# Kernel optimization log

Measured on AMD Instinct MI355X. Metric: run time of the kernel, lower is better.

## Reference

```python
import jax, jax.numpy as jnp
import numpy as np

B, S, D = 32, 1024, 1025  # batch, seq_length(=num_loci), input_dim
QD, KD = 64, 64
INIT_SCALE = 0.03


def _attention(y, Wq, Wk, Wv):
    # y: [B, S, D]
    q = jnp.einsum('bsd,dq->bsq', y, Wq)
    k = jnp.einsum('bsd,dk->bsk', y, Wk)
    v = jnp.einsum('bsd,de->bse', y, Wv)
    scores = jax.nn.softmax(jnp.einsum('bsq,btq->bst', q, k), axis=-1)
    return jnp.einsum('bst,bte->bse', scores, v)


def setup_inputs() -> dict:
    key = jax.random.key(0)
    ks = jax.random.split(key, 13)
    p = lambda k, shape: INIT_SCALE * jax.random.normal(k, shape, dtype=jnp.float32)
    return {
        'x': jax.random.normal(ks[0], (B, S, D), dtype=jnp.float32),
        'Wq1': p(ks[1], (D, QD)), 'Wk1': p(ks[2], (D, KD)), 'Wv1': p(ks[3], (D, D)),
        'Wq2': p(ks[4], (D, QD)), 'Wk2': p(ks[5], (D, KD)), 'Wv2': p(ks[6], (D, D)),
        'Wq3': p(ks[7], (D, QD)), 'Wk3': p(ks[8], (D, KD)), 'Wv3': p(ks[9], (D, D)),
        'random_matrix': p(ks[10], (S, D - 1)),
        'coeffs_attended': p(ks[11], (S, D)),
        'offset': p(ks[12], (1,)),
    }


def reference(x, Wq1, Wk1, Wv1, Wq2, Wk2, Wv2, Wq3, Wk3, Wv3,
              random_matrix, coeffs_attended, offset):
    # y = concat(x[:, :, :S] @ random_matrix, x[:, :, -1:])  -> [B, S, D]
    y = jnp.concatenate(
        [jnp.einsum('bsf,fe->bse', x[:, :, :S], random_matrix), x[:, :, -1:]],
        axis=2)
    a1 = _attention(y, Wq1, Wk1, Wv1)
    a2 = _attention(a1, Wq2, Wk2, Wv2)
    a3 = _attention(a2, Wq3, Wk3, Wv3)
    out = jnp.einsum('bij,ij->b', a3, coeffs_attended) + offset
    return out
```

## Files before the change

### kernel.cpp

```cpp
#include <hip/hip_runtime.h>
#include <hip/hip_bf16.h>
#include <stdint.h>

typedef __bf16 bf16;
typedef __bf16 bf16x8 __attribute__((ext_vector_type(8)));
typedef float f32x4 __attribute__((ext_vector_type(4)));
typedef float f32x8u __attribute__((ext_vector_type(8)));
typedef f32x8u f32x8a __attribute__((aligned(4)));

__device__ __forceinline__ void gl16(const void* g, void* lds) {
  __builtin_amdgcn_global_load_lds(
      (const __attribute__((address_space(1))) void*)g,
      (__attribute__((address_space(3))) void*)lds, 16, 0, 0);
}

template <int OUT>
__global__ __launch_bounds__(256) void gemm_hr(
    const bf16* __restrict__ Ah, const bf16* __restrict__ Ar, int lda,
    long long sA_, const bf16* __restrict__ Bh, const bf16* __restrict__ Br,
    int ldb, long long sB_, float* __restrict__ Cf, bf16* __restrict__ Ch,
    bf16* __restrict__ Cr, int ldc, long long sC_, int N, int K, int ntn) {
  __shared__ bf16 tAh[128][32], tAr[128][32], tBh[128][32], tBr[128][32];

  const int tid = threadIdx.x;
  const int lane = tid & 63, wave = tid >> 6;
  const int wm = wave & 1, wn = wave >> 1;
  const int fr = lane & 15, fq = lane >> 4;

  const long long bz = blockIdx.y;
  Ah += bz * sA_;
  Ar += bz * sA_;
  Bh += bz * sB_;
  Br += bz * sB_;

  const int cpx = gridDim.x >> 3;
  const int b2 = (blockIdx.x & 7) * cpx + (blockIdx.x >> 3);
  const int tm = b2 / ntn, tn = b2 % ntn;
  const int m0 = tm * 128, n0 = tn * 128;

  const int c0 = wave * 128 + lane;
  const int colsw = (((c0 & 3) ^ ((c0 >> 3) & 3)) << 3);
  const int rA0 = m0 + (c0 >> 2);
  int rB0 = n0 + (c0 >> 2), rB1 = rB0 + 16;
  rB0 = rB0 < N ? rB0 : N - 1;
  rB1 = rB1 < N ? rB1 : N - 1;
  const long long offA0 = (long long)rA0 * lda + colsw;
  const long long offA1 = offA0 + (long long)16 * lda;
  const long long offB0 = (long long)rB0 * ldb + colsw;
  const long long offB1 = (long long)rB1 * ldb + colsw;

  char* dAh = (char*)&tAh[0][0] + wave * 2048;
  char* dAr = (char*)&tAr[0][0] + wave * 2048;
  char* dBh = (char*)&tBh[0][0] + wave * 2048;
  char* dBr = (char*)&tBr[0][0] + wave * 2048;

  const int colA = ((fq ^ ((fr >> 1) & 3)) << 3);

  f32x4 acc[4][4] = {};
  const int nk = K >> 5;
  for (int kt = 0; kt < nk; ++kt) {
    const int k0 = kt << 5;
    gl16(Ah + offA0 + k0, dAh);
    gl16(Ah + offA1 + k0, dAh + 1024);
    gl16(Ar + offA0 + k0, dAr);
    gl16(Ar + offA1 + k0, dAr + 1024);
    gl16(Bh + offB0 + k0, dBh);
    gl16(Bh + offB1 + k0, dBh + 1024);
    gl16(Br + offB0 + k0, dBr);
    gl16(Br + offB1 + k0, dBr + 1024);
    __syncthreads();

    bf16x8 ah[4], ar_[4], bh[4], br_[4];
#pragma unroll
    for (int i = 0; i < 4; ++i) {
      ah[i] = *reinterpret_cast<const bf16x8*>(&tAh[wm * 64 + i * 16 + fr][colA]);
      ar_[i] = *reinterpret_cast<const bf16x8*>(&tAr[wm * 64 + i * 16 + fr][colA]);
      bh[i] = *reinterpret_cast<const bf16x8*>(&tBh[wn * 64 + i * 16 + fr][colA]);
      br_[i] = *reinterpret_cast<const bf16x8*>(&tBr[wn * 64 + i * 16 + fr][colA]);
    }
#pragma unroll
    for (int mi = 0; mi < 4; ++mi)
#pragma unroll
      for (int ni = 0; ni < 4; ++ni)
        acc[mi][ni] = __builtin_amdgcn_mfma_f32_16x16x32_bf16(
            ah[mi], bh[ni], acc[mi][ni], 0, 0, 0);
#pragma unroll
    for (int mi = 0; mi < 4; ++mi)
#pragma unroll
      for (int ni = 0; ni < 4; ++ni)
        acc[mi][ni] = __builtin_amdgcn_mfma_f32_16x16x32_bf16(
            ah[mi], br_[ni], acc[mi][ni], 0, 0, 0);
#pragma unroll
    for (int mi = 0; mi < 4; ++mi)
#pragma unroll
      for (int ni = 0; ni < 4; ++ni)
        acc[mi][ni] = __builtin_amdgcn_mfma_f32_16x16x32_bf16(
            ar_[mi], bh[ni], acc[mi][ni], 0, 0, 0);
    __syncthreads();
  }

  if constexpr (OUT == 0) {
    float* C = Cf + bz * sC_;
#pragma unroll
    for (int mi = 0; mi < 4; ++mi)
#pragma unroll
      for (int ni = 0; ni < 4; ++ni) {
        int cc = n0 + wn * 64 + ni * 16 + fr;
        if (cc < N) {
          long long base = (long long)(m0 + wm * 64 + mi * 16 + fq * 4) * ldc + cc;
#pragma unroll
          for (int j = 0; j < 4; ++j) C[base + (long long)j * ldc] = acc[mi][ni][j];
        }
      }
  } else {
    bf16* CH = Ch + bz * sC_;
    bf16* CR = Cr + bz * sC_;
#pragma unroll
    for (int mi = 0; mi < 4; ++mi)
#pragma unroll
      for (int ni = 0; ni < 4; ++ni) {
        int cc = n0 + wn * 64 + ni * 16 + fr;
        if (cc < N) {
          long long base = (long long)(m0 + wm * 64 + mi * 16 + fq * 4) * ldc + cc;
#pragma unroll
          for (int j = 0; j < 4; ++j) {
            float v = acc[mi][ni][j];
            bf16 h = (bf16)v;
            CH[base + (long long)j * ldc] = h;
            CR[base + (long long)j * ldc] = (bf16)(v - (float)h);
          }
        }
      }
  }
}

template <int OUT>
__global__ __launch_bounds__(256, 2) void gemm_hr2(
    const bf16* __restrict__ Ah, const bf16* __restrict__ Ar, int lda,
    long long sA_, const bf16* __restrict__ Bh, const bf16* __restrict__ Br,
    int ldb, long long sB_, float* __restrict__ Cf, bf16* __restrict__ Ch,
    bf16* __restrict__ Cr, int ldc, long long sC_, int N, int K, int ntn) {
  __shared__ bf16 tAh[256][32], tAr[256][32], tBh[128][32], tBr[128][32];

  const int tid = threadIdx.x;
  const int lane = tid & 63, wave = tid >> 6;
  const int wm = wave & 1, wn = wave >> 1;
  const int fr = lane & 15, fq = lane >> 4;

  const long long bz = blockIdx.y;
  Ah += bz * sA_;
  Ar += bz * sA_;
  Bh += bz * sB_;
  Br += bz * sB_;

  const int nwg = gridDim.x;
  const int q = nwg >> 3, r = nwg & 7;
  const int xcd = blockIdx.x & 7, o8 = blockIdx.x >> 3;
  const int b2 = (xcd < r ? xcd * (q + 1) : r * (q + 1) + (xcd - r) * q) + o8;
  const int tm = b2 / ntn, tn = b2 % ntn;
  const int m0 = tm * 256, n0 = tn * 128;

  const int cA = wave * 64 + lane;
  const int colsw = (((cA & 3) ^ ((cA >> 3) & 3)) << 3);
  const int rA = cA >> 2;
  const long long offA = (long long)(m0 + rA) * lda + colsw;
  const long long strA = (long long)64 * lda;
  int rB0 = n0 + rA, rB1 = n0 + rA + 64;
  rB0 = rB0 < N ? rB0 : N - 1;
  rB1 = rB1 < N ? rB1 : N - 1;
  const long long offB0 = (long long)rB0 * ldb + colsw;
  const long long offB1 = (long long)rB1 * ldb + colsw;

  char* dAh = (char*)&tAh[0][0] + wave * 1024;
  char* dAr = (char*)&tAr[0][0] + wave * 1024;
  char* dBh = (char*)&tBh[0][0] + wave * 1024;
  char* dBr = (char*)&tBr[0][0] + wave * 1024;

  const int colA = ((fq ^ ((fr >> 1) & 3)) << 3);

  f32x4 acc[8][4] = {};
  const int nk = K >> 5;
  for (int kt = 0; kt < nk; ++kt) {
    const int k0 = kt << 5;
#pragma unroll
    for (int j = 0; j < 4; ++j) {
      gl16(Ah + offA + j * strA + k0, dAh + j * 4096);
      gl16(Ar + offA + j * strA + k0, dAr + j * 4096);
    }
    gl16(Bh + offB0 + k0, dBh);
    gl16(Bh + offB1 + k0, dBh + 4096);
    gl16(Br + offB0 + k0, dBr);
    gl16(Br + offB1 + k0, dBr + 4096);
    __syncthreads();

    bf16x8 bh[4], br_[4];
#pragma unroll
    for (int i = 0; i < 4; ++i) {
      bh[i] = *reinterpret_cast<const bf16x8*>(&tBh[wn * 64 + i * 16 + fr][colA]);
      br_[i] = *reinterpret_cast<const bf16x8*>(&tBr[wn * 64 + i * 16 + fr][colA]);
    }
#pragma unroll
    for (int mi = 0; mi < 8; ++mi) {
      bf16x8 ah = *reinterpret_cast<const bf16x8*>(
          &tAh[wm * 128 + mi * 16 + fr][colA]);
      bf16x8 ar_ = *reinterpret_cast<const bf16x8*>(
          &tAr[wm * 128 + mi * 16 + fr][colA]);
#pragma unroll
      for (int ni = 0; ni < 4; ++ni)
        acc[mi][ni] = __builtin_amdgcn_mfma_f32_16x16x32_bf16(
            ah, bh[ni], acc[mi][ni], 0, 0, 0);
#pragma unroll
      for (int ni = 0; ni < 4; ++ni)
        acc[mi][ni] = __builtin_amdgcn_mfma_f32_16x16x32_bf16(
            ah, br_[ni], acc[mi][ni], 0, 0, 0);
#pragma unroll
      for (int ni = 0; ni < 4; ++ni)
        acc[mi][ni] = __builtin_amdgcn_mfma_f32_16x16x32_bf16(
            ar_, bh[ni], acc[mi][ni], 0, 0, 0);
    }
    __syncthreads();
  }

  if constexpr (OUT == 0) {
    float* C = Cf + bz * sC_;
#pragma unroll
    for (int mi = 0; mi < 8; ++mi)
#pragma unroll
      for (int ni = 0; ni < 4; ++ni) {
        int cc = n0 + wn * 64 + ni * 16 + fr;
        if (cc < N) {
          long long base =
              (long long)(m0 + wm * 128 + mi * 16 + fq * 4) * ldc + cc;
#pragma unroll
          for (int j = 0; j < 4; ++j) C[base + (long long)j * ldc] = acc[mi][ni][j];
        }
      }
  } else if constexpr (OUT == 1) {
    bf16* CH = Ch + bz * sC_;
    bf16* CR = Cr + bz * sC_;
#pragma unroll
    for (int mi = 0; mi < 8; ++mi)
#pragma unroll
      for (int ni = 0; ni < 4; ++ni) {
        int cc = n0 + wn * 64 + ni * 16 + fr;
        if (cc < N) {
          long long base =
              (long long)(m0 + wm * 128 + mi * 16 + fq * 4) * ldc + cc;
#pragma unroll
          for (int j = 0; j < 4; ++j) {
            float v = acc[mi][ni][j];
            bf16 h = (bf16)v;
            CH[base + (long long)j * ldc] = h;
            CR[base + (long long)j * ldc] = (bf16)(v - (float)h);
          }
        }
      }
  } else {
    bf16* CH = Ch + bz * sC_;
    bf16* CR = Cr + bz * sC_;
#pragma unroll
    for (int mi = 0; mi < 8; ++mi)
#pragma unroll
      for (int ni = 0; ni < 4; ++ni) {
        int cc = n0 + wn * 64 + ni * 16 + fr;
        if (cc < N) {
          int mr = m0 + wm * 128 + mi * 16 + fq * 4;
          union { bf16 h[4]; uint2 u; } th, tr;
#pragma unroll
          for (int j = 0; j < 4; ++j) {
            float v = acc[mi][ni][j];
            bf16 h = (bf16)v;
            th.h[j] = h;
            tr.h[j] = (bf16)(v - (float)h);
          }
          *reinterpret_cast<uint2*>(CH + (long long)cc * ldc + mr) = th.u;
          *reinterpret_cast<uint2*>(CR + (long long)cc * ldc + mr) = tr.u;
        }
      }
  }
}

__global__ __launch_bounds__(256, 2) void gemm_dot1(
    const bf16* __restrict__ Ah, int lda, long long sA_,
    const bf16* __restrict__ Bh, int ldb, long long sB_, int N, int K,
    int ntn, const float* __restrict__ G, int ldg,
    float* __restrict__ partial) {
  __shared__ bf16 tAh[256][32], tBh[128][32];

  const int tid = threadIdx.x;
  const int lane = tid & 63, wave = tid >> 6;
  const int wm = wave & 1, wn = wave >> 1;
  const int fr = lane & 15, fq = lane >> 4;

  const long long bz = blockIdx.y;
  Ah += bz * sA_;
  Bh += bz * sB_;

  const int nwg = gridDim.x;
  const int q = nwg >> 3, r = nwg & 7;
  const int xcd = blockIdx.x & 7, o8 = blockIdx.x >> 3;
  const int b2 = (xcd < r ? xcd * (q + 1) : r * (q + 1) + (xcd - r) * q) + o8;
  const int tm = b2 / ntn, tn = b2 % ntn;
  const int m0 = tm * 256, n0 = tn * 128;

  const int cA = wave * 64 + lane;
  const int colsw = (((cA & 3) ^ ((cA >> 3) & 3)) << 3);
  const int rA = cA >> 2;
  const long long offA = (long long)(m0 + rA) * lda + colsw;
  const long long strA = (long long)64 * lda;
  int rB0 = n0 + rA, rB1 = n0 + rA + 64;
  rB0 = rB0 < N ? rB0 : N - 1;
  rB1 = rB1 < N ? rB1 : N - 1;
  const long long offB0 = (long long)rB0 * ldb + colsw;
  const long long offB1 = (long long)rB1 * ldb + colsw;

  char* dAh = (char*)&tAh[0][0] + wave * 1024;
  char* dBh = (char*)&tBh[0][0] + wave * 1024;

  const int colA = ((fq ^ ((fr >> 1) & 3)) << 3);

  f32x4 acc[8][4] = {};
  const int nk = K >> 5;
  for (int kt = 0; kt < nk; ++kt) {
    const int k0 = kt << 5;
#pragma unroll
    for (int j = 0; j < 4; ++j) gl16(Ah + offA + j * strA + k0, dAh + j * 4096);
    gl16(Bh + offB0 + k0, dBh);
    gl16(Bh + offB1 + k0, dBh + 4096);
    __syncthreads();

    bf16x8 bh[4];
#pragma unroll
    for (int i = 0; i < 4; ++i)
      bh[i] = *reinterpret_cast<const bf16x8*>(&tBh[wn * 64 + i * 16 + fr][colA]);
#pragma unroll
    for (int mi = 0; mi < 8; ++mi) {
      bf16x8 ah = *reinterpret_cast<const bf16x8*>(
          &tAh[wm * 128 + mi * 16 + fr][colA]);
#pragma unroll
      for (int ni = 0; ni < 4; ++ni)
        acc[mi][ni] = __builtin_amdgcn_mfma_f32_16x16x32_bf16(
            ah, bh[ni], acc[mi][ni], 0, 0, 0);
    }
    __syncthreads();
  }

  float dot = 0.f;
#pragma unroll
  for (int mi = 0; mi < 8; ++mi)
#pragma unroll
    for (int ni = 0; ni < 4; ++ni) {
      int cc = n0 + wn * 64 + ni * 16 + fr;
      if (cc < N) {
        long long base =
            (long long)(m0 + wm * 128 + mi * 16 + fq * 4) * ldg + cc;
#pragma unroll
        for (int j = 0; j < 4; ++j)
          dot += acc[mi][ni][j] * G[base + (long long)j * ldg];
      }
    }
#pragma unroll
  for (int o = 32; o; o >>= 1) dot += __shfl_xor(dot, o);
  float* red = (float*)&tAh[0][0];
  if (lane == 0) red[wave] = dot;
  __syncthreads();
  if (tid == 0)
    partial[bz * gridDim.x + b2] = red[0] + red[1] + red[2] + red[3];
}

__global__ __launch_bounds__(256) void gemm0_split(
    const float* __restrict__ A, int lda, const float* __restrict__ B, int ldb,
    bf16* __restrict__ Ch, bf16* __restrict__ Cr, int ldc, int N, int K,
    int ntn) {
  __shared__ bf16 tAh[128][32], tAr[128][32], tBh[128][32], tBr[128][32];

  const int tid = threadIdx.x;
  const int lane = tid & 63, wave = tid >> 6;
  const int wm = wave & 1, wn = wave >> 1;
  const int fr = lane & 15, fq = lane >> 4;

  const int cpx = gridDim.x >> 3;
  const int b2 = (blockIdx.x & 7) * cpx + (blockIdx.x >> 3);
  const int tm = b2 / ntn, tn = b2 % ntn;
  const int m0 = tm * 128, n0 = tn * 128;

  const int row0 = tid >> 2, slot = tid & 3;
  const int wcol = ((slot ^ ((tid >> 3) & 3)) << 3);
  const int colA = ((fq ^ ((fr >> 1) & 3)) << 3);

  f32x4 acc[4][4] = {};
  const int nk = K >> 5;
  for (int kt = 0; kt < nk; ++kt) {
    const int k0 = kt << 5;
    f32x8a ra[2], rb[2];
#pragma unroll
    for (int p = 0; p < 2; ++p) {
      int row = row0 + p * 64;
      ra[p] = *reinterpret_cast<const f32x8a*>(
          A + (long long)(m0 + row) * lda + k0 + slot * 8);
      int n = n0 + row;
      n = n < N ? n : N - 1;
      rb[p] = *reinterpret_cast<const f32x8a*>(
          B + (long long)n * ldb + k0 + slot * 8);
    }
    __syncthreads();
#pragma unroll
    for (int p = 0; p < 2; ++p) {
      int row = row0 + p * 64;
      bf16x8 ah, arr, bhh, brr;
#pragma unroll
      for (int j = 0; j < 8; ++j) {
        float fa = ra[p][j], fb = rb[p][j];
        bf16 ha = (bf16)fa, hb = (bf16)fb;
        ah[j] = ha;
        arr[j] = (bf16)(fa - (float)ha);
        bhh[j] = hb;
        brr[j] = (bf16)(fb - (float)hb);
      }
      *reinterpret_cast<bf16x8*>(&tAh[row][wcol]) = ah;
      *reinterpret_cast<bf16x8*>(&tAr[row][wcol]) = arr;
      *reinterpret_cast<bf16x8*>(&tBh[row][wcol]) = bhh;
      *reinterpret_cast<bf16x8*>(&tBr[row][wcol]) = brr;
    }
    __syncthreads();

    bf16x8 ah[4], ar_[4], bh[4], br_[4];
#pragma unroll
    for (int i = 0; i < 4; ++i) {
      ah[i] = *reinterpret_cast<const bf16x8*>(&tAh[wm * 64 + i * 16 + fr][colA]);
      ar_[i] = *reinterpret_cast<const bf16x8*>(&tAr[wm * 64 + i * 16 + fr][colA]);
      bh[i] = *reinterpret_cast<const bf16x8*>(&tBh[wn * 64 + i * 16 + fr][colA]);
      br_[i] = *reinterpret_cast<const bf16x8*>(&tBr[wn * 64 + i * 16 + fr][colA]);
    }
#pragma unroll
    for (int mi = 0; mi < 4; ++mi)
#pragma unroll
      for (int ni = 0; ni < 4; ++ni)
        acc[mi][ni] = __builtin_amdgcn_mfma_f32_16x16x32_bf16(
            ah[mi], bh[ni], acc[mi][ni], 0, 0, 0);
#pragma unroll
    for (int mi = 0; mi < 4; ++mi)
#pragma unroll
      for (int ni = 0; ni < 4; ++ni)
        acc[mi][ni] = __builtin_amdgcn_mfma_f32_16x16x32_bf16(
            ah[mi], br_[ni], acc[mi][ni], 0, 0, 0);
#pragma unroll
    for (int mi = 0; mi < 4; ++mi)
#pragma unroll
      for (int ni = 0; ni < 4; ++ni)
        acc[mi][ni] = __builtin_amdgcn_mfma_f32_16x16x32_bf16(
            ar_[mi], bh[ni], acc[mi][ni], 0, 0, 0);
  }

#pragma unroll
  for (int mi = 0; mi < 4; ++mi)
#pragma unroll
    for (int ni = 0; ni < 4; ++ni) {
      int cc = n0 + wn * 64 + ni * 16 + fr;
      if (cc < N) {
        long long base = (long long)(m0 + wm * 64 + mi * 16 + fq * 4) * ldc + cc;
#pragma unroll
        for (int j = 0; j < 4; ++j) {
          float v = acc[mi][ni][j];
          bf16 h = (bf16)v;
          Ch[base + (long long)j * ldc] = h;
          Cr[base + (long long)j * ldc] = (bf16)(v - (float)h);
        }
      }
    }
}

template <int SPLIT>
__global__ __launch_bounds__(256) void transpose_tile(
    const float* __restrict__ src, int R, int Cc, float* __restrict__ df,
    bf16* __restrict__ dh, bf16* __restrict__ dr, int Nout, int outC,
    int ntk) {
  __shared__ float t[32][33];
  const int nt = blockIdx.x / ntk, kt = blockIdx.x % ntk;
  const int n0 = nt * 32, k0 = kt * 32;
  const int c = threadIdx.x & 31, r0 = threadIdx.x >> 5;
#pragma unroll
  for (int p = 0; p < 4; ++p) {
    int k = k0 + r0 + p * 8, n = n0 + c;
    t[r0 + p * 8][c] = (k < R && n < Cc) ? src[(long long)k * Cc + n] : 0.f;
  }
  __syncthreads();
#pragma unroll
  for (int p = 0; p < 4; ++p) {
    int n = n0 + r0 + p * 8, k = k0 + c;
    if (n < Nout && k < outC) {
      float v = t[c][r0 + p * 8];
      long long idx = (long long)n * outC + k;
      if constexpr (SPLIT) {
        bf16 h = (bf16)v;
        dh[idx] = h;
        dr[idx] = (bf16)(v - (float)h);
      } else {
        df[idx] = v;
      }
    }
  }
}

__global__ __launch_bounds__(256) void transpose_h(
    const ushort* __restrict__ sh, ushort* __restrict__ dh) {
  __shared__ ushort lh[32][33];
  const long long b = blockIdx.y;
  const int et = blockIdx.x >> 5, tt = blockIdx.x & 31;
  const int e0 = et * 32, t0 = tt * 32;
  const int c = threadIdx.x & 31, r0 = threadIdx.x >> 5;
  const ushort* sh_b = sh + b * 1024 * 1056;
#pragma unroll
  for (int p = 0; p < 4; ++p) {
    int t = t0 + r0 + p * 8;
    lh[r0 + p * 8][c] = sh_b[(long long)t * 1056 + e0 + c];
  }
  __syncthreads();
  ushort* dh_b = dh + b * 1056 * 1024;
#pragma unroll
  for (int p = 0; p < 4; ++p) {
    int e = e0 + r0 + p * 8;
    dh_b[(long long)e * 1024 + t0 + c] = lh[c][r0 + p * 8];
  }
}

__global__ __launch_bounds__(256) void pad_split_g(
    const float* __restrict__ src, int R, int Cc, bf16* __restrict__ dh,
    bf16* __restrict__ dr, long long total, int outC) {
  long long idx = (long long)blockIdx.x * 256 + threadIdx.x;
  if (idx >= total) return;
  int n = (int)(idx / outC), k = (int)(idx % outC);
  float v = (n < R && k < Cc) ? src[(long long)n * Cc + k] : 0.f;
  bf16 h = (bf16)v;
  dh[idx] = h;
  dr[idx] = (bf16)(v - (float)h);
}

__global__ __launch_bounds__(256) void fixup_y_split(bf16* __restrict__ Yh,
                                                     bf16* __restrict__ Yr,
                                                     const float* __restrict__ x) {
  int row = blockIdx.x * 256 + threadIdx.x;
  if (row < 32768) {
    float v = x[(long long)row * 1025 + 1024];
    bf16 h = (bf16)v;
    long long base = (long long)row * 1056;
    Yh[base + 1024] = h;
    Yr[base + 1024] = (bf16)(v - (float)h);
#pragma unroll
    for (int c = 1025; c < 1056; ++c) {
      Yh[base + c] = (bf16)0.f;
      Yr[base + c] = (bf16)0.f;
    }
  }
}

__global__ __launch_bounds__(256) void softmax_split(
    const float* __restrict__ Plog, bf16* __restrict__ Ph,
    bf16* __restrict__ Pr, int wr) {
  long long row = blockIdx.x;
  const float* p = Plog + row * 1024;
  int tid = threadIdx.x;
  float v[4];
#pragma unroll
  for (int j = 0; j < 4; ++j) v[j] = p[tid + 256 * j];
  float m = fmaxf(fmaxf(v[0], v[1]), fmaxf(v[2], v[3]));
#pragma unroll
  for (int o = 32; o; o >>= 1) m = fmaxf(m, __shfl_xor(m, o));
  __shared__ float sm[4];
  if ((tid & 63) == 0) sm[tid >> 6] = m;
  __syncthreads();
  m = fmaxf(fmaxf(sm[0], sm[1]), fmaxf(sm[2], sm[3]));
  float s = 0.f;
#pragma unroll
  for (int j = 0; j < 4; ++j) {
    v[j] = __expf(v[j] - m);
    s += v[j];
  }
#pragma unroll
  for (int o = 32; o; o >>= 1) s += __shfl_xor(s, o);
  __shared__ float ss[4];
  if ((tid & 63) == 0) ss[tid >> 6] = s;
  __syncthreads();
  s = ss[0] + ss[1] + ss[2] + ss[3];
  float inv = 1.0f / s;
#pragma unroll
  for (int j = 0; j < 4; ++j) {
    float pv = v[j] * inv;
    bf16 h = (bf16)pv;
    Ph[row * 1024 + tid + 256 * j] = h;
    if (wr) Pr[row * 1024 + tid + 256 * j] = (bf16)(pv - (float)h);
  }
}

__global__ void finalize_k(const float* __restrict__ partial,
                           const float* __restrict__ offs,
                           float* __restrict__ out, int per_b) {
  int b = threadIdx.x;
  if (b < 32) {
    float s = 0.f;
    for (int i = 0; i < per_b; ++i) s += partial[b * per_b + i];
    out[b] = s + offs[0];
  }
}


extern "C" void kernel_launch(void* const* d_in, const int* in_sizes, int n_in,
                              void* d_out, int out_size, void* d_ws,
                              size_t ws_size, hipStream_t stream) {
  const float* x = (const float*)d_in[0];
  const float* Wq[3] = {(const float*)d_in[1], (const float*)d_in[4],
                        (const float*)d_in[7]};
  const float* Wk[3] = {(const float*)d_in[2], (const float*)d_in[5],
                        (const float*)d_in[8]};
  const float* Wv[3] = {(const float*)d_in[3], (const float*)d_in[6],
                        (const float*)d_in[9]};
  const float* R = (const float*)d_in[10];
  const float* coef = (const float*)d_in[11];
  const float* offs = (const float*)d_in[12];
  float* out = (float*)d_out;

  const int CB = (ws_size >= (size_t)390000000ULL) ? 16 : 8;
  const int NCH = 32 / CB;

  char* ws = (char*)d_ws;
  size_t off = 0;
  auto alloc = [&](size_t bytes) -> void* {
    void* p = ws + off;
    off = (off + bytes + 255) & ~(size_t)255;
    return p;
  };
  bf16* Yh = (bf16*)alloc(32768LL * 1056 * 2);
  bf16* Yr = (bf16*)alloc(32768LL * 1056 * 2);
  bf16* qkh = (bf16*)alloc(32768LL * 128 * 2);
  bf16* qkr = (bf16*)alloc(32768LL * 128 * 2);
  float* Plog = (float*)alloc((long long)CB * 1024 * 1024 * 4);
  bf16* Ph = (bf16*)alloc((long long)CB * 1024 * 1024 * 2);
  bf16* Pr = (bf16*)alloc((long long)CB * 1024 * 1024 * 2);
  bf16* vTh = (bf16*)alloc((long long)CB * 1056 * 1024 * 2);
  bf16* vTr = (bf16*)alloc((long long)CB * 1056 * 1024 * 2);
  float* RT = (float*)alloc(1024LL * 1024 * 4);
  bf16 *WqkTh[3], *WqkTr[3], *WvTh[3], *WvTr[3];
  for (int i = 0; i < 3; ++i) {
    WqkTh[i] = (bf16*)alloc(128LL * 1056 * 2);
    WqkTr[i] = (bf16*)alloc(128LL * 1056 * 2);
    WvTh[i] = (bf16*)alloc(1056LL * 1056 * 2);
    WvTr[i] = (bf16*)alloc(1056LL * 1056 * 2);
  }
  bf16* coefh = (bf16*)alloc(1024LL * 1056 * 2);
  bf16* coefr = (bf16*)alloc(1024LL * 1056 * 2);
  float* G = (float*)alloc(1024LL * 1056 * 4);
  float* partial = (float*)alloc(32 * 36 * 4);

  transpose_tile<0><<<32 * 32, 256, 0, stream>>>(R, 1024, 1024, RT, nullptr,
                                                 nullptr, 1024, 1024, 32);
  for (int l = 0; l < 3; ++l) {
    transpose_tile<1><<<33 * 2, 256, 0, stream>>>(
        Wq[l], 1025, 64, nullptr, WqkTh[l], WqkTr[l], 64, 1056, 33);
    transpose_tile<1><<<33 * 2, 256, 0, stream>>>(
        Wk[l], 1025, 64, nullptr, WqkTh[l] + 64 * 1056, WqkTr[l] + 64 * 1056,
        64, 1056, 33);
    if (l < 2) {
      transpose_tile<1><<<33 * 33, 256, 0, stream>>>(
          Wv[l], 1025, 1025, nullptr, WvTh[l], WvTr[l], 1056, 1056, 33);
    } else {
      pad_split_g<<<4356, 256, 0, stream>>>(Wv[l], 1025, 1025, WvTh[l],
                                            WvTr[l], 1056LL * 1056, 1056);
    }
  }
  pad_split_g<<<4224, 256, 0, stream>>>(coef, 1024, 1025, coefh, coefr,
                                        1024LL * 1056, 1056);
  gemm_hr<0><<<dim3(72, 1), 256, 0, stream>>>(
      coefh, coefr, 1056, 0, WvTh[2], WvTr[2], 1056, 0, G, nullptr, nullptr,
      1056, 0, 1056, 1056, 9);

  gemm0_split<<<dim3(2048, 1), 256, 0, stream>>>(x, 1025, RT, 1024, Yh, Yr,
                                                 1056, 1024, 1024, 8);
  fixup_y_split<<<128, 256, 0, stream>>>(Yh, Yr, x);

  for (int l = 0; l < 3; ++l) {
    gemm_hr<1><<<dim3(256, 1), 256, 0, stream>>>(
        Yh, Yr, 1056, 0, WqkTh[l], WqkTr[l], 1056, 0, nullptr, qkh, qkr, 128,
        0, 128, 1056, 1);
    for (int ch = 0; ch < NCH; ++ch) {
      const long long b0 = (long long)ch * CB;
      bf16* Ych = Yh + b0 * 1024 * 1056;
      bf16* Ycr = Yr + b0 * 1024 * 1056;
      bf16* qkch = qkh + b0 * 1024 * 128;
      bf16* qkcr = qkr + b0 * 1024 * 128;
      if (l < 2) {
        gemm_hr2<2><<<dim3(36, CB), 256, 0, stream>>>(
            Ych, Ycr, 1056, 1024LL * 1056, WvTh[l], WvTr[l], 1056, 0, nullptr,
            vTh, vTr, 1024, 1056LL * 1024, 1056, 1056, 9);
      } else {
        transpose_h<<<dim3(33 * 32, CB), 256, 0, stream>>>(
            (const ushort*)Ych, (ushort*)vTh);
      }
      gemm_hr2<0><<<dim3(32, CB), 256, 0, stream>>>(
          qkch, qkcr, 128, 1024LL * 128, qkch + 64, qkcr + 64, 128,
          1024LL * 128, Plog, nullptr, nullptr, 1024, 1024LL * 1024, 1024, 64,
          8);
      softmax_split<<<CB * 1024, 256, 0, stream>>>(Plog, Ph, Pr, l < 2 ? 1 : 0);
      if (l < 2) {
        gemm_hr2<1><<<dim3(36, CB), 256, 0, stream>>>(
            Ph, Pr, 1024, 1024LL * 1024, vTh, vTr, 1024, 1056LL * 1024,
            nullptr, Ych, Ycr, 1056, 1024LL * 1056, 1056, 1024, 9);
      } else {
        gemm_dot1<<<dim3(36, CB), 256, 0, stream>>>(
            Ph, 1024, 1024LL * 1024, vTh, 1024, 1056LL * 1024, 1056, 1024, 9,
            G, 1056, partial + b0 * 36);
      }
    }
  }

  finalize_k<<<1, 32, 0, stream>>>(partial, offs, out, 36);
}
```

Baseline: 2.332 ms.

## Fuse exp into score GEMM epilogue and defer softmax normalization to PV GEMM

The score GEMM epilogue now applies exp directly and writes bf16 hi/lo probabilities, dropping the fp32 logits buffer and the separate max/exp/normalize softmax pass. A lightweight row-sum kernel computes reciprocal sums, which are applied in the epilogues of the following PV GEMM and the final dot kernel. The QK projection switches to the larger 256-row tile kernel, and the workspace threshold for the larger batch chunk is lowered because the logits buffer is gone. Skipping max subtraction relies on the score magnitudes staying small enough not to overflow exp, and row sums are taken from the rounded bf16 high part only.

```diff
diff --git a/kernel.cpp b/kernel.cpp
--- a/kernel.cpp
+++ b/kernel.cpp
@@ -139,7 +139,8 @@
     const bf16* __restrict__ Ah, const bf16* __restrict__ Ar, int lda,
     long long sA_, const bf16* __restrict__ Bh, const bf16* __restrict__ Br,
     int ldb, long long sB_, float* __restrict__ Cf, bf16* __restrict__ Ch,
-    bf16* __restrict__ Cr, int ldc, long long sC_, int N, int K, int ntn) {
+    bf16* __restrict__ Cr, int ldc, long long sC_, int N, int K, int ntn,
+    const float* __restrict__ Rinv) {
   __shared__ bf16 tAh[256][32], tAr[256][32], tBh[128][32], tBr[128][32];
 
   const int tid = threadIdx.x;
@@ -238,24 +239,26 @@
   } else if constexpr (OUT == 1) {
     bf16* CH = Ch + bz * sC_;
     bf16* CR = Cr + bz * sC_;
+    const float* rz = Rinv ? Rinv + bz * 1024 : nullptr;
 #pragma unroll
     for (int mi = 0; mi < 8; ++mi)
 #pragma unroll
       for (int ni = 0; ni < 4; ++ni) {
         int cc = n0 + wn * 64 + ni * 16 + fr;
         if (cc < N) {
-          long long base =
-              (long long)(m0 + wm * 128 + mi * 16 + fq * 4) * ldc + cc;
+          int gr = m0 + wm * 128 + mi * 16 + fq * 4;
+          long long base = (long long)gr * ldc + cc;
 #pragma unroll
           for (int j = 0; j < 4; ++j) {
             float v = acc[mi][ni][j];
+            if (rz) v *= rz[gr + j];
             bf16 h = (bf16)v;
             CH[base + (long long)j * ldc] = h;
             CR[base + (long long)j * ldc] = (bf16)(v - (float)h);
           }
         }
       }
-  } else {
+  } else if constexpr (OUT == 2) {
     bf16* CH = Ch + bz * sC_;
     bf16* CR = Cr + bz * sC_;
 #pragma unroll
@@ -277,6 +280,26 @@
           *reinterpret_cast<uint2*>(CR + (long long)cc * ldc + mr) = tr.u;
         }
       }
+  } else {
+    bf16* CH = Ch + bz * sC_;
+    bf16* CR = Cr ? Cr + bz * sC_ : nullptr;
+#pragma unroll
+    for (int mi = 0; mi < 8; ++mi)
+#pragma unroll
+      for (int ni = 0; ni < 4; ++ni) {
+        int cc = n0 + wn * 64 + ni * 16 + fr;
+        if (cc < N) {
+          long long base =
+              (long long)(m0 + wm * 128 + mi * 16 + fq * 4) * ldc + cc;
+#pragma unroll
+          for (int j = 0; j < 4; ++j) {
+            float v = __expf(acc[mi][ni][j]);
+            bf16 h = (bf16)v;
+            CH[base + (long long)j * ldc] = h;
+            if (CR) CR[base + (long long)j * ldc] = (bf16)(v - (float)h);
+          }
+        }
+      }
   }
 }
 
@@ -284,7 +307,7 @@
     const bf16* __restrict__ Ah, int lda, long long sA_,
     const bf16* __restrict__ Bh, int ldb, long long sB_, int N, int K,
     int ntn, const float* __restrict__ G, int ldg,
-    float* __restrict__ partial) {
+    const float* __restrict__ Rinv, float* __restrict__ partial) {
   __shared__ bf16 tAh[256][32], tBh[128][32];
 
   const int tid = threadIdx.x;
@@ -295,6 +318,7 @@
   const long long bz = blockIdx.y;
   Ah += bz * sA_;
   Bh += bz * sB_;
+  const float* rz = Rinv + bz * 1024;
 
   const int nwg = gridDim.x;
   const int q = nwg >> 3, r = nwg & 7;
@@ -352,11 +376,11 @@
     for (int ni = 0; ni < 4; ++ni) {
       int cc = n0 + wn * 64 + ni * 16 + fr;
       if (cc < N) {
-        long long base =
-            (long long)(m0 + wm * 128 + mi * 16 + fq * 4) * ldg + cc;
+        int gr = m0 + wm * 128 + mi * 16 + fq * 4;
+        long long base = (long long)gr * ldg + cc;
 #pragma unroll
         for (int j = 0; j < 4; ++j)
-          dot += acc[mi][ni][j] * G[base + (long long)j * ldg];
+          dot += acc[mi][ni][j] * rz[gr + j] * G[base + (long long)j * ldg];
       }
     }
 #pragma unroll
@@ -554,42 +578,20 @@
   }
 }
 
-__global__ __launch_bounds__(256) void softmax_split(
-    const float* __restrict__ Plog, bf16* __restrict__ Ph,
-    bf16* __restrict__ Pr, int wr) {
+__global__ __launch_bounds__(256) void rowsum_k(const bf16* __restrict__ Eh,
+                                                float* __restrict__ rinv) {
   long long row = blockIdx.x;
-  const float* p = Plog + row * 1024;
+  const bf16* p = Eh + row * 1024;
   int tid = threadIdx.x;
-  float v[4];
-#pragma unroll
-  for (int j = 0; j < 4; ++j) v[j] = p[tid + 256 * j];
-  float m = fmaxf(fmaxf(v[0], v[1]), fmaxf(v[2], v[3]));
-#pragma unroll
-  for (int o = 32; o; o >>= 1) m = fmaxf(m, __shfl_xor(m, o));
-  __shared__ float sm[4];
-  if ((tid & 63) == 0) sm[tid >> 6] = m;
-  __syncthreads();
-  m = fmaxf(fmaxf(sm[0], sm[1]), fmaxf(sm[2], sm[3]));
   float s = 0.f;
 #pragma unroll
-  for (int j = 0; j < 4; ++j) {
-    v[j] = __expf(v[j] - m);
-    s += v[j];
-  }
+  for (int j = 0; j < 4; ++j) s += (float)p[tid + 256 * j];
 #pragma unroll
   for (int o = 32; o; o >>= 1) s += __shfl_xor(s, o);
   __shared__ float ss[4];
   if ((tid & 63) == 0) ss[tid >> 6] = s;
   __syncthreads();
-  s = ss[0] + ss[1] + ss[2] + ss[3];
-  float inv = 1.0f / s;
-#pragma unroll
-  for (int j = 0; j < 4; ++j) {
-    float pv = v[j] * inv;
-    bf16 h = (bf16)pv;
-    Ph[row * 1024 + tid + 256 * j] = h;
-    if (wr) Pr[row * 1024 + tid + 256 * j] = (bf16)(pv - (float)h);
-  }
+  if (tid == 0) rinv[row] = 1.0f / (ss[0] + ss[1] + ss[2] + ss[3]);
 }
 
 __global__ void finalize_k(const float* __restrict__ partial,
@@ -619,7 +621,7 @@
   const float* offs = (const float*)d_in[12];
   float* out = (float*)d_out;
 
-  const int CB = (ws_size >= (size_t)390000000ULL) ? 16 : 8;
+  const int CB = (ws_size >= (size_t)340000000ULL) ? 16 : 8;
   const int NCH = 32 / CB;
 
   char* ws = (char*)d_ws;
@@ -633,11 +635,11 @@
   bf16* Yr = (bf16*)alloc(32768LL * 1056 * 2);
   bf16* qkh = (bf16*)alloc(32768LL * 128 * 2);
   bf16* qkr = (bf16*)alloc(32768LL * 128 * 2);
-  float* Plog = (float*)alloc((long long)CB * 1024 * 1024 * 4);
   bf16* Ph = (bf16*)alloc((long long)CB * 1024 * 1024 * 2);
   bf16* Pr = (bf16*)alloc((long long)CB * 1024 * 1024 * 2);
   bf16* vTh = (bf16*)alloc((long long)CB * 1056 * 1024 * 2);
   bf16* vTr = (bf16*)alloc((long long)CB * 1056 * 1024 * 2);
+  float* rinv = (float*)alloc((long long)CB * 1024 * 4);
   float* RT = (float*)alloc(1024LL * 1024 * 4);
   bf16 *WqkTh[3], *WqkTr[3], *WvTh[3], *WvTr[3];
   for (int i = 0; i < 3; ++i) {
@@ -678,9 +680,9 @@
   fixup_y_split<<<128, 256, 0, stream>>>(Yh, Yr, x);
 
   for (int l = 0; l < 3; ++l) {
-    gemm_hr<1><<<dim3(256, 1), 256, 0, stream>>>(
+    gemm_hr2<1><<<dim3(128, 1), 256, 0, stream>>>(
         Yh, Yr, 1056, 0, WqkTh[l], WqkTr[l], 1056, 0, nullptr, qkh, qkr, 128,
-        0, 128, 1056, 1);
+        0, 128, 1056, 1, nullptr);
     for (int ch = 0; ch < NCH; ++ch) {
       const long long b0 = (long long)ch * CB;
       bf16* Ych = Yh + b0 * 1024 * 1056;
@@ -690,24 +692,24 @@
       if (l < 2) {
         gemm_hr2<2><<<dim3(36, CB), 256, 0, stream>>>(
             Ych, Ycr, 1056, 1024LL * 1056, WvTh[l], WvTr[l], 1056, 0, nullptr,
-            vTh, vTr, 1024, 1056LL * 1024, 1056, 1056, 9);
+            vTh, vTr, 1024, 1056LL * 1024, 1056, 1056, 9, nullptr);
       } else {
         transpose_h<<<dim3(33 * 32, CB), 256, 0, stream>>>(
             (const ushort*)Ych, (ushort*)vTh);
       }
-      gemm_hr2<0><<<dim3(32, CB), 256, 0, stream>>>(
+      gemm_hr2<4><<<dim3(32, CB), 256, 0, stream>>>(
           qkch, qkcr, 128, 1024LL * 128, qkch + 64, qkcr + 64, 128,
-          1024LL * 128, Plog, nullptr, nullptr, 1024, 1024LL * 1024, 1024, 64,
-          8);
-      softmax_split<<<CB * 1024, 256, 0, stream>>>(Plog, Ph, Pr, l < 2 ? 1 : 0);
+          1024LL * 128, nullptr, Ph, (l < 2) ? Pr : nullptr, 1024,
+          1024LL * 1024, 1024, 64, 8, nullptr);
+      rowsum_k<<<CB * 1024, 256, 0, stream>>>(Ph, rinv);
       if (l < 2) {
         gemm_hr2<1><<<dim3(36, CB), 256, 0, stream>>>(
             Ph, Pr, 1024, 1024LL * 1024, vTh, vTr, 1024, 1056LL * 1024,
-            nullptr, Ych, Ycr, 1056, 1024LL * 1056, 1056, 1024, 9);
+            nullptr, Ych, Ycr, 1056, 1024LL * 1056, 1056, 1024, 9, rinv);
       } else {
         gemm_dot1<<<dim3(36, CB), 256, 0, stream>>>(
             Ph, 1024, 1024LL * 1024, vTh, 1024, 1056LL * 1024, 1056, 1024, 9,
-            G, 1056, partial + b0 * 36);
+            G, 1056, rinv, partial + b0 * 36);
       }
     }
   }
```

New measurement: 2.424 ms. +3.9%, slower.
